# Optimization experiments

Hardware: AMD Instinct MI355X
Metric: run time of the kernel (lower is better)

Reference implementation:

```python
import jax, jax.numpy as jnp
import numpy as np

VOCAB = 8192
EMB = 80
UNITS = 2048
LAYERS = 6
BATCH = 64
SEQ = 64


def setup_inputs() -> dict:
    key = jax.random.key(0)
    ks = jax.random.split(key, 7)
    inputs = jax.random.randint(ks[0], (BATCH, SEQ), 0, VOCAB)
    emb = jax.random.normal(ks[1], (VOCAB, EMB), dtype=jnp.float32) * 0.05
    Wx = jax.random.normal(ks[2], (LAYERS, EMB, UNITS), dtype=jnp.float32) / np.sqrt(EMB)
    Wh = jax.random.normal(ks[3], (LAYERS, UNITS, UNITS), dtype=jnp.float32) / np.sqrt(UNITS)
    b = jnp.zeros((LAYERS, UNITS), dtype=jnp.float32)
    Wout = jax.random.normal(ks[4], (UNITS, 1), dtype=jnp.float32) / np.sqrt(UNITS)
    bout = jnp.zeros((1,), dtype=jnp.float32)
    return {"inputs": inputs, "emb": emb, "Wx": Wx, "Wh": Wh, "b": b, "Wout": Wout, "bout": bout}


def reference(inputs, emb, Wx, Wh, b, Wout, bout):
    # x: [B, T, EMB]
    x = emb[inputs]
    L = Wx.shape[0]
    B, U = inputs.shape[0], Wh.shape[-1]

    def step(states, xt):
        # states: [L, B, U]; xt: [B, EMB]
        # Faithful to original: every layer consumes xt and states[0],
        # and states[0] is updated before layers 1..L-1 read it.
        s0 = states[0]
        hs = []
        for i in range(L):
            h = jnp.tanh(xt @ Wx[i] + s0 @ Wh[i] + b[i])
            if i == 0:
                s0 = h
            hs.append(h)
        return jnp.stack(hs), None

    init = jnp.zeros((L, B, U), dtype=x.dtype)
    states, _ = jax.lax.scan(step, init, jnp.swapaxes(x, 0, 1))
    h_last = states[-1]  # last layer's output at final timestep, [B, U]
    return jax.nn.sigmoid(h_last @ Wout + bout)
```

## Files before the change

kernel.cpp:

```cpp
#include <hip/hip_runtime.h>
#include <math.h>

#define VOCABN 8192
#define EMBN   80
#define UNITSN 2048
#define BATCHN 64
#define SEQN   64

typedef _Float16 f16;
typedef _Float16 f16x8 __attribute__((ext_vector_type(8)));
typedef float    f32x4 __attribute__((ext_vector_type(4)));
typedef unsigned int u32x2 __attribute__((ext_vector_type(2)));

#define BROW 4352

#define HBUF_BYTES   (2 * 4 * 64 * 1024)
#define FLAGS_OFF    HBUF_BYTES
#define OUTPRE_OFF   (FLAGS_OFF + 4 * 64 * 4)
#define WS_ZERO_B    (OUTPRE_OFF + BATCHN * 4)

#define KPW 544

__device__ __forceinline__ f32x4 mfma16(f16x8 a, f16x8 b, f32x4 c) {
    return __builtin_amdgcn_mfma_f32_16x16x32_f16(a, b, c, 0, 0, 0);
}

__device__ __forceinline__ void bypass_load_b16(f16x8* dst, const void* p) {
    asm volatile("global_load_dwordx4 %0, %1, off sc0 sc1"
                 : "=v"(*dst) : "v"(p) : "memory");
}
__device__ __forceinline__ int bypass_load_b32(const void* p) {
    int r;
    asm volatile("global_load_dword %0, %1, off sc0 sc1\n\ts_waitcnt vmcnt(0)"
                 : "=v"(r) : "v"(p) : "memory");
    return r;
}
__device__ __forceinline__ void bypass_store_b32(void* p, unsigned int v) {
    asm volatile("global_store_dword %0, %1, off sc0 sc1"
                 :: "v"(p), "v"(v) : "memory");
}
__device__ __forceinline__ void bypass_store_b64(void* p, u32x2 v) {
    asm volatile("global_store_dwordx2 %0, %1, off sc0 sc1"
                 :: "v"(p), "v"(v) : "memory");
}
__device__ __forceinline__ void wait_vm0(void) {
    asm volatile("s_waitcnt vmcnt(0)" ::: "memory");
    __builtin_amdgcn_sched_barrier(0);
}
__device__ __forceinline__ unsigned int us(f16 h) {
    return (unsigned int)__builtin_bit_cast(unsigned short, h);
}

__global__ __launch_bounds__(256, 1)
void rnn_recur(const int* __restrict__ inputs, const float* __restrict__ emb,
               const float* __restrict__ Wx, const float* __restrict__ Wh,
               const float* __restrict__ bias, f16* __restrict__ hbuf,
               int* __restrict__ flags)
{
    __shared__ __align__(16) char smem[99840];
    __shared__ f16  xlds[2][16][96];
    __shared__ int  idxlds[16][SEQN];

    const int tid = threadIdx.x;
    const int wg  = blockIdx.x;
    const int g     = wg >> 5;
    const int wslot = wg & 31;
    const int c0  = wslot * 64;
    const int g16 = g * 16;

    for (int i = tid; i < 16 * SEQN; i += 256)
        idxlds[i >> 6][i & 63] = inputs[(g16 + (i >> 6)) * SEQN + (i & 63)];

    const int lane = tid & 63;
    const int wv   = tid >> 6;
    const int l16  = lane & 15;
    const int lq   = lane >> 4;

    f16x8 b[17][4];
    {
        f16* Wtmp = (f16*)smem;
        for (int ch = 0; ch < 3; ++ch) {
            const int base  = ch * 768;
            const int nrows = (base + 768 <= 2176) ? 768 : (2176 - base);
            for (int rp = 0; rp < nrows; rp += 16) {
                const int r_ = rp + (tid >> 4);
                if (r_ < nrows) {
                    const int k = base + r_;
                    float4 w = {0.f, 0.f, 0.f, 0.f};
                    if (k < UNITSN)
                        w = *(const float4*)(Wh + (size_t)k * UNITSN + c0 + (tid & 15) * 4);
                    else if (k - UNITSN < EMBN)
                        w = *(const float4*)(Wx + (size_t)(k - UNITSN) * UNITSN + c0 + (tid & 15) * 4);
                    f16* d = &Wtmp[r_ * 65 + (tid & 15) * 4];
                    d[0] = (f16)w.x; d[1] = (f16)w.y; d[2] = (f16)w.z; d[3] = (f16)w.w;
                }
            }
            __syncthreads();
#pragma unroll
            for (int i = 0; i < 17; ++i) {
                const int k = wv * KPW + i * 32;
                if (k >= base && k < base + 768) {
                    const int kl = k - base + lq * 8;
#pragma unroll
                    for (int ct = 0; ct < 4; ++ct) {
#pragma unroll
                        for (int e = 0; e < 8; ++e)
                            b[i][ct][e] = Wtmp[(kl + e) * 65 + ct * 16 + l16];
                    }
                }
            }
            __syncthreads();
        }
    }

    {
        const int r  = tid >> 4;
        const int kb = (tid & 15) * 6;
        const float* erow = emb + (size_t)idxlds[r][0] * EMBN;
#pragma unroll
        for (int q = 0; q < 6; ++q) {
            const int k = kb + q;
            xlds[0][r][k] = (f16)((k < EMBN) ? erow[k] : 0.f);
        }
    }
    __syncthreads();

    const int rr = tid >> 4;
    const int cb = (tid & 15) * 4;
    float bias4[4];
#pragma unroll
    for (int q = 0; q < 4; ++q) bias4[q] = bias[c0 + cb + q];
    const int gc     = c0 + cb;
    const int kt_p   = gc >> 5;
    const int cc     = gc & 31;
    const int lane_t = ((cc >> 3) << 4) | rr;
    const int pbyte  = lane_t * 16 + (cc & 7) * 2;

    char* hb = (char*)hbuf;
    int* gflags = flags + g * 32;
    float* red = (float*)smem;

    for (int t = 0; t < SEQN; ++t) {
        const int p = t & 1;

        f32x4 acc[4];
#pragma unroll
        for (int ct = 0; ct < 4; ++ct) acc[ct] = (f32x4){0.f, 0.f, 0.f, 0.f};
        {
            const char* hsrc = hb + ((p * 4 + g) << 16) + (lane << 4);
            f16x8 av[17];
#pragma unroll
            for (int i = 0; i < 17; ++i) {
                if (wv * KPW + i * 32 < UNITSN)
                    bypass_load_b16(&av[i], hsrc + ((wv * 17 + i) << 10));
            }
            f16x8 axf0 = {}, axf1 = {}, axf2 = {};
            if (wv == 3) {
                axf0 = *(const f16x8*)(&xlds[p][l16][0 * 32 + lq * 8]);
                axf1 = *(const f16x8*)(&xlds[p][l16][1 * 32 + lq * 8]);
                axf2 = *(const f16x8*)(&xlds[p][l16][2 * 32 + lq * 8]);
            }
            wait_vm0();
#pragma unroll
            for (int i = 0; i < 17; ++i) {
                if (wv * KPW + i * 32 < UNITSN) {
#pragma unroll
                    for (int ct = 0; ct < 4; ++ct)
                        acc[ct] = mfma16(av[i], b[i][ct], acc[ct]);
                }
            }
            if (wv == 3) {
#pragma unroll
                for (int ct = 0; ct < 4; ++ct) acc[ct] = mfma16(axf0, b[13][ct], acc[ct]);
#pragma unroll
                for (int ct = 0; ct < 4; ++ct) acc[ct] = mfma16(axf1, b[14][ct], acc[ct]);
#pragma unroll
                for (int ct = 0; ct < 4; ++ct) acc[ct] = mfma16(axf2, b[15][ct], acc[ct]);
            }
        }
#pragma unroll
        for (int ct = 0; ct < 4; ++ct)
            *(f32x4*)(&red[(((wv * 4) + ct) * 64 + lane) * 4]) = acc[ct];
        __syncthreads();

        {
            float vv[4];
#pragma unroll
            for (int q = 0; q < 4; ++q) {
                const int c  = cb + q;
                const int tl = c >> 4;
                const int la = ((rr >> 2) << 4) | (c & 15);
                const int rg = rr & 3;
                float s = bias4[q];
#pragma unroll
                for (int w = 0; w < 4; ++w)
                    s += red[(((w * 4) + tl) * 64 + la) * 4 + rg];
                vv[q] = tanhf(s);
            }
            u32x2 pk;
            pk[0] = us((f16)vv[0]) | (us((f16)vv[1]) << 16);
            pk[1] = us((f16)vv[2]) | (us((f16)vv[3]) << 16);
            char* dst = hb + ((((t + 1) & 1) * 4 + g) << 16) + (kt_p << 10) + pbyte;
            bypass_store_b64(dst, pk);
        }
        asm volatile("s_waitcnt vmcnt(0)" ::: "memory");
        __syncthreads();

        if (t == SEQN - 1) break;

        if (tid == 0)
            bypass_store_b32(&gflags[wslot], (unsigned int)(t + 1));

        {
            const int r  = tid >> 4;
            const int kb = (tid & 15) * 6;
            const float* erow = emb + (size_t)idxlds[r][t + 1] * EMBN;
            const int buf = (t + 1) & 1;
#pragma unroll
            for (int q = 0; q < 6; ++q) {
                const int k = kb + q;
                xlds[buf][r][k] = (f16)((k < EMBN) ? erow[k] : 0.f);
            }
        }

        if (wv == 0) {
            int tries = 0;
            for (;;) {
                const int v = bypass_load_b32(&gflags[lane & 31]);
                if (__all(v > t)) break;
                __builtin_amdgcn_s_sleep(1);
                if (++tries > 150000) break;
            }
        }
        __syncthreads();
    }
}

__device__ __forceinline__ void load_wslice(const float* __restrict__ W,
                                            const float* __restrict__ Wxp,
                                            int c0, int tid, unsigned char* Blds)
{
    const int j0 = tid >> 3, l8 = tid & 7;
    for (int it = 0; it < 64; ++it) {
        const int j = j0 + it * 32;
        const float4 w = *(const float4*)(W + (size_t)j * UNITSN + c0 + l8 * 4);
        const float vals[4] = {w.x, w.y, w.z, w.w};
#pragma unroll
        for (int q = 0; q < 4; ++q) {
            const int uu = l8 * 4 + q;
            *(f16*)(Blds + uu * BROW + ((2 * j) ^ ((uu & 15) << 4))) = (f16)vals[q];
        }
    }
    for (int j2 = j0; j2 < 96; j2 += 32) {
        float vals[4] = {0.f, 0.f, 0.f, 0.f};
        if (j2 < EMBN) {
            const float4 w = *(const float4*)(Wxp + (size_t)j2 * UNITSN + c0 + l8 * 4);
            vals[0] = w.x; vals[1] = w.y; vals[2] = w.z; vals[3] = w.w;
        }
#pragma unroll
        for (int q = 0; q < 4; ++q) {
            const int uu = l8 * 4 + q;
            const int k = 2048 + j2;
            *(f16*)(Blds + uu * BROW + ((2 * k) ^ ((uu & 15) << 4))) = (f16)vals[q];
        }
    }
}

__global__ __launch_bounds__(256)
void final_gemm(const int* __restrict__ inputs, const float* __restrict__ emb,
                const float* __restrict__ Wx, const float* __restrict__ Wh,
                const float* __restrict__ bias, const float* __restrict__ Wout,
                const f16* __restrict__ hbuf, float* __restrict__ out_pre)
{
    __shared__ unsigned char Blds[32 * BROW];
    __shared__ f16  xlds[64][96];
    __shared__ float red[4][64][4];
    __shared__ float rowacc[64][4];

    const int tid = threadIdx.x;
    const int c0  = blockIdx.x * 32;
    const float* Wh5 = Wh + (size_t)5 * UNITSN * UNITSN;
    const float* Wx5 = Wx + (size_t)5 * EMBN * UNITSN;
    const float* b5  = bias + 5 * UNITSN;
    const char* hb = (const char*)hbuf;

    load_wslice(Wh5, Wx5, c0, tid, Blds);
    {
        const int r  = tid >> 2;
        const int kb = (tid & 3) * 24;
        const float* erow = emb + (size_t)inputs[r * SEQN + SEQN - 1] * EMBN;
#pragma unroll
        for (int q = 0; q < 24; ++q) {
            const int k = kb + q;
            xlds[r][k] = (f16)((k < EMBN) ? erow[k] : 0.f);
        }
    }
    rowacc[tid >> 2][tid & 3] = 0.f;
    __syncthreads();

    const int lane = tid & 63;
    const int wv   = tid >> 6;
    const int l16  = lane & 15;
    const int lq   = lane >> 4;

    for (int ct = 0; ct < 2; ++ct) {
        f32x4 acc[4];
#pragma unroll
        for (int rt = 0; rt < 4; ++rt) acc[rt] = (f32x4){0.f, 0.f, 0.f, 0.f};
        const unsigned char* brow = Blds + (ct * 16 + l16) * BROW;
        const int swz = l16 << 4;
#pragma unroll
        for (int rt = 0; rt < 4; ++rt) {
            const char* hsrc = hb + (rt << 16) + (lane << 4);
            f16x8 av[16];
#pragma unroll
            for (int kk = 0; kk < 16; ++kk)
                av[kk] = *(const f16x8*)(hsrc + ((wv * 16 + kk) << 10));
            f16x8 ax;
            if (wv < 3) ax = *(const f16x8*)(&xlds[rt * 16 + l16][wv * 32 + lq * 8]);
#pragma unroll
            for (int kk = 0; kk < 16; ++kk) {
                const int k0 = wv * 512 + kk * 32 + lq * 8;
                acc[rt] = mfma16(av[kk], *(const f16x8*)(brow + ((2 * k0) ^ swz)), acc[rt]);
            }
            if (wv < 3) {
                const int k0 = 2048 + wv * 32 + lq * 8;
                acc[rt] = mfma16(ax, *(const f16x8*)(brow + ((2 * k0) ^ swz)), acc[rt]);
            }
        }
        if (wv == 0) {
#pragma unroll
            for (int rt = 0; rt < 4; ++rt) *(f32x4*)(&red[rt][lane][0]) = acc[rt];
        }
        __syncthreads();
#pragma unroll
        for (int w = 1; w < 4; ++w) {
            if (wv == w) {
#pragma unroll
                for (int rt = 0; rt < 4; ++rt) {
                    f32x4 cur = *(f32x4*)(&red[rt][lane][0]);
                    cur += acc[rt];
                    *(f32x4*)(&red[rt][lane][0]) = cur;
                }
            }
            __syncthreads();
        }
        {
            const int r = tid >> 2;
            float rsum = 0.f;
#pragma unroll
            for (int q = 0; q < 4; ++q) {
                const int cl = (tid & 3) * 4 + q;
                const int c  = ct * 16 + cl;
                const int lidx = (((r & 15) >> 2) << 4) + cl;
                float v = red[r >> 4][lidx][r & 3] + b5[c0 + c];
                v = tanhf(v);
                rsum += v * Wout[c0 + c];
            }
            rowacc[r][tid & 3] += rsum;
        }
        __syncthreads();
    }
    if (tid < 64) {
        const float s = rowacc[tid][0] + rowacc[tid][1] + rowacc[tid][2] + rowacc[tid][3];
        atomicAdd(&out_pre[tid], s);
    }
}

__global__ void final_out(const float* __restrict__ out_pre,
                          const float* __restrict__ bout, float* __restrict__ out)
{
    const int b = threadIdx.x;
    if (b < BATCHN) out[b] = 1.f / (1.f + expf(-(out_pre[b] + bout[0])));
}

extern "C" void kernel_launch(void* const* d_in, const int* in_sizes, int n_in,
                              void* d_out, int out_size, void* d_ws, size_t ws_size,
                              hipStream_t stream) {
    (void)in_sizes; (void)n_in; (void)out_size; (void)ws_size;
    const int*   inputs = (const int*)d_in[0];
    const float* emb    = (const float*)d_in[1];
    const float* Wx     = (const float*)d_in[2];
    const float* Wh     = (const float*)d_in[3];
    const float* bias   = (const float*)d_in[4];
    const float* Wout   = (const float*)d_in[5];
    const float* bout   = (const float*)d_in[6];
    float* out = (float*)d_out;

    f16*   hbuf    = (f16*)d_ws;
    int*   flags   = (int*)((char*)d_ws + FLAGS_OFF);
    float* out_pre = (float*)((char*)d_ws + OUTPRE_OFF);

    (void)hipMemsetAsync(d_ws, 0, WS_ZERO_B, stream);

    hipStreamCaptureStatus cs = hipStreamCaptureStatusNone;
    (void)hipStreamIsCapturing(stream, &cs);
    if (cs == hipStreamCaptureStatusActive) {
        rnn_recur<<<dim3(128), dim3(256), 0, stream>>>(inputs, emb, Wx, Wh, bias, hbuf, flags);
    } else {
        void* args[] = {(void*)&inputs, (void*)&emb, (void*)&Wx, (void*)&Wh,
                        (void*)&bias, (void*)&hbuf, (void*)&flags};
        hipError_t e = hipLaunchCooperativeKernel((const void*)rnn_recur, dim3(128), dim3(256),
                                                  args, 0, stream);
        if (e != hipSuccess) {
            rnn_recur<<<dim3(128), dim3(256), 0, stream>>>(inputs, emb, Wx, Wh, bias, hbuf, flags);
        }
    }
    final_gemm<<<dim3(64), dim3(256), 0, stream>>>(inputs, emb, Wx, Wh, bias, Wout, hbuf, out_pre);
    final_out<<<dim3(1), dim3(64), 0, stream>>>(out_pre, bout, out);
}
```

Measured before the change: 344.5 us.

## Replace flag-based inter-block barrier with parity bits embedded in hidden-state data

Removes the per-step flag store, the flag polling loop and one extra barrier. Readiness is instead encoded in the low mantissa bit of each fp16 hidden value, alternating parity every two steps. Consumers poll the hidden-state tiles directly and reload only chunks that are not yet ready. This cuts one round-trip of global-memory latency per timestep, at the cost of losing one mantissa bit of precision and of repeated polling loads of the full tile. The second hbuf parity half is pre-filled with 0x01 so the first wait resolves correctly.

```diff
diff --git a/kernel.cpp b/kernel.cpp
--- a/kernel.cpp
+++ b/kernel.cpp
@@ -11,12 +11,14 @@
 typedef _Float16 f16x8 __attribute__((ext_vector_type(8)));
 typedef float    f32x4 __attribute__((ext_vector_type(4)));
 typedef unsigned int u32x2 __attribute__((ext_vector_type(2)));
+typedef unsigned int u32x4 __attribute__((ext_vector_type(4)));
 
 #define BROW 4352
 
 #define HBUF_BYTES   (2 * 4 * 64 * 1024)
+#define PAR_BYTES    (4 * 64 * 1024)
 #define FLAGS_OFF    HBUF_BYTES
-#define OUTPRE_OFF   (FLAGS_OFF + 4 * 64 * 4)
+#define OUTPRE_OFF   (FLAGS_OFF + 256 * 4)
 #define WS_ZERO_B    (OUTPRE_OFF + BATCHN * 4)
 
 #define KPW 544
@@ -28,16 +30,6 @@
 __device__ __forceinline__ void bypass_load_b16(f16x8* dst, const void* p) {
     asm volatile("global_load_dwordx4 %0, %1, off sc0 sc1"
                  : "=v"(*dst) : "v"(p) : "memory");
-}
-__device__ __forceinline__ int bypass_load_b32(const void* p) {
-    int r;
-    asm volatile("global_load_dword %0, %1, off sc0 sc1\n\ts_waitcnt vmcnt(0)"
-                 : "=v"(r) : "v"(p) : "memory");
-    return r;
-}
-__device__ __forceinline__ void bypass_store_b32(void* p, unsigned int v) {
-    asm volatile("global_store_dword %0, %1, off sc0 sc1"
-                 :: "v"(p), "v"(v) : "memory");
 }
 __device__ __forceinline__ void bypass_store_b64(void* p, u32x2 v) {
     asm volatile("global_store_dwordx2 %0, %1, off sc0 sc1"
@@ -57,6 +49,7 @@
                const float* __restrict__ bias, f16* __restrict__ hbuf,
                int* __restrict__ flags)
 {
+    (void)flags;
     __shared__ __align__(16) char smem[99840];
     __shared__ f16  xlds[2][16][96];
     __shared__ int  idxlds[16][SEQN];
@@ -67,6 +60,7 @@
     const int wslot = wg & 31;
     const int c0  = wslot * 64;
     const int g16 = g * 16;
+    (void)wslot;
 
     for (int i = tid; i < 16 * SEQN; i += 256)
         idxlds[i >> 6][i & 63] = inputs[(g16 + (i >> 6)) * SEQN + (i & 63)];
@@ -137,30 +131,53 @@
     const int pbyte  = lane_t * 16 + (cc & 7) * 2;
 
     char* hb = (char*)hbuf;
-    int* gflags = flags + g * 32;
     float* red = (float*)smem;
+
+    unsigned all_mask = 0;
+#pragma unroll
+    for (int i = 0; i < 17; ++i)
+        if (wv * KPW + i * 32 < UNITSN) all_mask |= (1u << i);
 
     for (int t = 0; t < SEQN; ++t) {
         const int p = t & 1;
+        const unsigned int eM = ((t >> 1) & 1) ? 0x00010001u : 0u;
+
+        f16x8 av[17];
+        const char* hsrc = hb + ((p * 4 + g) << 16) + (lane << 4);
+        unsigned rdy = 0;
+        int tries = 0;
+        for (;;) {
+#pragma unroll
+            for (int i = 0; i < 17; ++i)
+                if ((wv * KPW + i * 32 < UNITSN) && !((rdy >> i) & 1))
+                    bypass_load_b16(&av[i], hsrc + ((wv * 17 + i) << 10));
+            wait_vm0();
+#pragma unroll
+            for (int i = 0; i < 17; ++i) {
+                if ((wv * KPW + i * 32 < UNITSN) && !((rdy >> i) & 1)) {
+                    const u32x4 d = __builtin_bit_cast(u32x4, av[i]);
+                    const bool ok = ((d[0] & 0x00010001u) == eM)
+                                 && ((d[1] & 0x00010001u) == eM)
+                                 && ((d[2] & 0x00010001u) == eM)
+                                 && ((d[3] & 0x00010001u) == eM);
+                    if (__all(ok)) rdy |= (1u << i);
+                }
+            }
+            if ((rdy & all_mask) == all_mask) break;
+            if (++tries > 30000) break;
+            __builtin_amdgcn_s_sleep(1);
+        }
 
         f32x4 acc[4];
 #pragma unroll
         for (int ct = 0; ct < 4; ++ct) acc[ct] = (f32x4){0.f, 0.f, 0.f, 0.f};
         {
-            const char* hsrc = hb + ((p * 4 + g) << 16) + (lane << 4);
-            f16x8 av[17];
-#pragma unroll
-            for (int i = 0; i < 17; ++i) {
-                if (wv * KPW + i * 32 < UNITSN)
-                    bypass_load_b16(&av[i], hsrc + ((wv * 17 + i) << 10));
-            }
             f16x8 axf0 = {}, axf1 = {}, axf2 = {};
             if (wv == 3) {
                 axf0 = *(const f16x8*)(&xlds[p][l16][0 * 32 + lq * 8]);
                 axf1 = *(const f16x8*)(&xlds[p][l16][1 * 32 + lq * 8]);
                 axf2 = *(const f16x8*)(&xlds[p][l16][2 * 32 + lq * 8]);
             }
-            wait_vm0();
 #pragma unroll
             for (int i = 0; i < 17; ++i) {
                 if (wv * KPW + i * 32 < UNITSN) {
@@ -184,6 +201,7 @@
         __syncthreads();
 
         {
+            const unsigned int ebM = (((t + 1) >> 1) & 1) ? 0x00010001u : 0u;
             float vv[4];
 #pragma unroll
             for (int q = 0; q < 4; ++q) {
@@ -198,20 +216,13 @@
                 vv[q] = tanhf(s);
             }
             u32x2 pk;
-            pk[0] = us((f16)vv[0]) | (us((f16)vv[1]) << 16);
-            pk[1] = us((f16)vv[2]) | (us((f16)vv[3]) << 16);
+            pk[0] = ((us((f16)vv[0]) & 0xFFFEu) | ((us((f16)vv[1]) & 0xFFFEu) << 16)) | ebM;
+            pk[1] = ((us((f16)vv[2]) & 0xFFFEu) | ((us((f16)vv[3]) & 0xFFFEu) << 16)) | ebM;
             char* dst = hb + ((((t + 1) & 1) * 4 + g) << 16) + (kt_p << 10) + pbyte;
             bypass_store_b64(dst, pk);
         }
-        asm volatile("s_waitcnt vmcnt(0)" ::: "memory");
-        __syncthreads();
-
-        if (t == SEQN - 1) break;
-
-        if (tid == 0)
-            bypass_store_b32(&gflags[wslot], (unsigned int)(t + 1));
-
-        {
+
+        if (t < SEQN - 1) {
             const int r  = tid >> 4;
             const int kb = (tid & 15) * 6;
             const float* erow = emb + (size_t)idxlds[r][t + 1] * EMBN;
@@ -220,16 +231,6 @@
             for (int q = 0; q < 6; ++q) {
                 const int k = kb + q;
                 xlds[buf][r][k] = (f16)((k < EMBN) ? erow[k] : 0.f);
-            }
-        }
-
-        if (wv == 0) {
-            int tries = 0;
-            for (;;) {
-                const int v = bypass_load_b32(&gflags[lane & 31]);
-                if (__all(v > t)) break;
-                __builtin_amdgcn_s_sleep(1);
-                if (++tries > 150000) break;
             }
         }
         __syncthreads();
@@ -391,7 +392,9 @@
     int*   flags   = (int*)((char*)d_ws + FLAGS_OFF);
     float* out_pre = (float*)((char*)d_ws + OUTPRE_OFF);
 
-    (void)hipMemsetAsync(d_ws, 0, WS_ZERO_B, stream);
+    (void)hipMemsetAsync(d_ws, 0x00, PAR_BYTES, stream);
+    (void)hipMemsetAsync((char*)d_ws + PAR_BYTES, 0x01, PAR_BYTES, stream);
+    (void)hipMemsetAsync((char*)d_ws + HBUF_BYTES, 0x00, WS_ZERO_B - HBUF_BYTES, stream);
 
     hipStreamCaptureStatus cs = hipStreamCaptureStatusNone;
     (void)hipStreamIsCapturing(stream, &cs);
```

New measurement: 427.7 us. +24.2%, slower.
